# Kernel tuning notes

Hardware: AMD Instinct MI355X
Metric: run time of the kernel (lower is better)

## Reference

```python
import jax, jax.numpy as jnp
import numpy as np

N_NODES = 50000
N_EDGES = 1600000
NODE_DIM = 1024
HID = 128
OUT = 128
LN_EPS = 1e-5


def setup_inputs() -> dict:
    key = jax.random.key(0)
    ks = jax.random.split(key, 8)
    s = lambda d: 1.0 / np.sqrt(d)
    return {
        "x": jax.random.normal(ks[0], (N_NODES, NODE_DIM), jnp.float32),
        "edge_index": jax.random.randint(ks[1], (2, N_EDGES), 0, N_NODES, jnp.int64),
        "proj_w": jax.random.normal(ks[2], (HID, NODE_DIM), jnp.float32) * s(NODE_DIM),
        "proj_b": jnp.zeros((HID,), jnp.float32),
        "lin_l_w": jax.random.normal(ks[3], (HID, HID), jnp.float32) * s(HID),
        "lin_l_b": jnp.zeros((HID,), jnp.float32),
        "lin_r_w": jax.random.normal(ks[4], (HID, HID), jnp.float32) * s(HID),
        "ln_g": jnp.ones((HID,), jnp.float32),
        "ln_b": jnp.zeros((HID,), jnp.float32),
        "out_w": jax.random.normal(ks[5], (OUT, HID), jnp.float32) * s(HID),
        "out_b": jnp.zeros((OUT,), jnp.float32),
    }


def reference(x, edge_index, proj_w, proj_b, lin_l_w, lin_l_b, lin_r_w, ln_g, ln_b, out_w, out_b):
    n = x.shape[0]
    # input projection + ReLU: [N, node_dim] -> [N, H]
    h = jax.nn.relu(x @ proj_w.T + proj_b)
    # SAGEConv(mean): gather source features, mean-scatter to targets
    src, dst = edge_index[0], edge_index[1]
    agg = jax.ops.segment_sum(h[src], dst, num_segments=n)  # [N, H]
    deg = jax.ops.segment_sum(jnp.ones((src.shape[0],), h.dtype), dst, num_segments=n)
    mean_nbr = agg / jnp.maximum(deg, 1.0)[:, None]
    h = mean_nbr @ lin_l_w.T + lin_l_b + h @ lin_r_w.T
    # LayerNorm over feature dim
    mu = h.mean(-1, keepdims=True)
    var = jnp.mean((h - mu) ** 2, -1, keepdims=True)
    h = (h - mu) * jax.lax.rsqrt(var + LN_EPS) * ln_g + ln_b
    h = jax.nn.relu(h)  # dropout is identity in eval
    # batch=None -> global mean pool over all nodes: [1, H]
    g = h.mean(0, keepdims=True)
    return g @ out_w.T + out_b
```

## Files before the change

### kernel.cpp

```cpp
#include <hip/hip_runtime.h>

#define N_NODES  50000
#define N_EDGES  1600000
#define NODE_DIM 1024
#define HID      128
#define LN_EPS   1e-5f
#define PAD_NODES 50176
#define NBUCK    196
#define SHARD    6250

typedef float f32x4 __attribute__((ext_vector_type(4)));
typedef __bf16 bf16x8 __attribute__((ext_vector_type(8)));
typedef unsigned short u16x8 __attribute__((ext_vector_type(8)));

__device__ __forceinline__ unsigned short f2bf(float f) {
  unsigned int u = __float_as_uint(f);
  u += 0x7fffu + ((u >> 16) & 1u);
  return (unsigned short)(u >> 16);
}
__device__ __forceinline__ float bf2f(unsigned short v) {
  return __uint_as_float((unsigned int)v << 16);
}

__device__ __forceinline__ void pack16(const float4 v0, const float4 v1,
                                       const float4 v2, const float4 v3,
                                       unsigned short* dst) {
  u16x8 p0 = {f2bf(v0.x), f2bf(v0.y), f2bf(v0.z), f2bf(v0.w),
              f2bf(v1.x), f2bf(v1.y), f2bf(v1.z), f2bf(v1.w)};
  u16x8 p1 = {f2bf(v2.x), f2bf(v2.y), f2bf(v2.z), f2bf(v2.w),
              f2bf(v3.x), f2bf(v3.y), f2bf(v3.z), f2bf(v3.w)};
  *(u16x8*)(dst)     = p0;
  *(u16x8*)(dst + 8) = p1;
}

__device__ __forceinline__ int scan256_excl(int v, int buf[2][256], int t) {
  int cur = 0;
  buf[0][t] = v;
  __syncthreads();
  for (int off = 1; off < 256; off <<= 1) {
    int nxt = cur ^ 1;
    int s = buf[cur][t];
    if (t >= off) s += buf[cur][t - off];
    buf[nxt][t] = s;
    cur = nxt;
    __syncthreads();
  }
  return buf[cur][t] - v;
}

__global__ __launch_bounds__(256) void k_proj(const float* __restrict__ x,
                                              const float* __restrict__ pw,
                                              const float* __restrict__ pb,
                                              unsigned short* __restrict__ h) {
  __shared__ unsigned short As[128 * 32];
  __shared__ unsigned short Bs[128 * 32];
  const int tid  = threadIdx.x;
  const int m0   = blockIdx.x * 128;
  const int wave = tid >> 6, lane = tid & 63;
  const int wm = (wave >> 1) * 64, wn = (wave & 1) * 64;
  const int srow = tid >> 1;
  const int scol = (tid & 1) * 16;
  const int fr = lane & 15, ko = (lane >> 4) * 8;

  f32x4 acc[4][4];
#pragma unroll
  for (int m = 0; m < 4; m++)
#pragma unroll
    for (int n = 0; n < 4; n++) acc[m][n] = (f32x4){0.f, 0.f, 0.f, 0.f};

  for (int k0 = 0; k0 < NODE_DIM; k0 += 32) {
    const int arow = m0 + srow;
    float4 a0, a1, a2, a3;
    if (arow < N_NODES) {
      const float4* p = (const float4*)(x + (size_t)arow * NODE_DIM + k0 + scol);
      a0 = p[0]; a1 = p[1]; a2 = p[2]; a3 = p[3];
    } else {
      a0 = a1 = a2 = a3 = make_float4(0.f, 0.f, 0.f, 0.f);
    }
    const float4* q = (const float4*)(pw + (size_t)srow * NODE_DIM + k0 + scol);
    float4 b0 = q[0], b1 = q[1], b2 = q[2], b3 = q[3];

    __syncthreads();
    pack16(a0, a1, a2, a3, &As[srow * 32 + scol]);
    pack16(b0, b1, b2, b3, &Bs[srow * 32 + scol]);
    __syncthreads();

    bf16x8 af[4], bfr[4];
#pragma unroll
    for (int m = 0; m < 4; m++)
      af[m] = *(const bf16x8*)&As[(wm + m * 16 + fr) * 32 + ko];
#pragma unroll
    for (int n = 0; n < 4; n++)
      bfr[n] = *(const bf16x8*)&Bs[(wn + n * 16 + fr) * 32 + ko];
#pragma unroll
    for (int m = 0; m < 4; m++)
#pragma unroll
      for (int n = 0; n < 4; n++)
        acc[m][n] = __builtin_amdgcn_mfma_f32_16x16x32_bf16(af[m], bfr[n], acc[m][n], 0, 0, 0);
  }

  const int cr = (lane >> 4) * 4, cc = lane & 15;
#pragma unroll
  for (int n = 0; n < 4; n++) {
    const int col = wn + n * 16 + cc;
    const float bias = pb[col];
#pragma unroll
    for (int m = 0; m < 4; m++) {
#pragma unroll
      for (int i = 0; i < 4; i++) {
        const int row = m0 + wm + m * 16 + cr + i;
        if (row < N_NODES) {
          float v = acc[m][n][i] + bias;
          h[(size_t)row * HID + col] = f2bf(v > 0.f ? v : 0.f);
        }
      }
    }
  }
}

__global__ __launch_bounds__(256) void k_hist(const int* __restrict__ ei,
                                              int* __restrict__ counts) {
  __shared__ int bins[NBUCK];
  int t = threadIdx.x;
  if (t < NBUCK) bins[t] = 0;
  __syncthreads();
  int base = blockIdx.x * SHARD;
  for (int i = t; i < SHARD; i += 256)
    atomicAdd(&bins[ei[N_EDGES + base + i] >> 8], 1);
  __syncthreads();
  if (t < NBUCK) counts[t * 256 + blockIdx.x] = bins[t];
}

__global__ __launch_bounds__(256) void k_s1(const int* __restrict__ counts,
                                            int* __restrict__ basem,
                                            int* __restrict__ btot) {
  __shared__ int buf[2][256];
  int t = threadIdx.x, b = blockIdx.x;
  int v = counts[b * 256 + t];
  int excl = scan256_excl(v, buf, t);
  basem[b * 256 + t] = excl;
  if (t == 255) btot[b] = excl + v;
}

__global__ __launch_bounds__(256) void k_s2(const int* __restrict__ btot,
                                            int* __restrict__ bstart,
                                            float* __restrict__ accum) {
  __shared__ int buf[2][256];
  int t = threadIdx.x;
  int v = (t < NBUCK) ? btot[t] : 0;
  int excl = scan256_excl(v, buf, t);
  if (t < NBUCK) bstart[t] = excl;
  if (t == 0) bstart[NBUCK] = N_EDGES;
  if (t < HID) accum[t] = 0.f;
}

__global__ __launch_bounds__(256) void k_scatter(const int* __restrict__ ei,
                                                 const int* __restrict__ basem,
                                                 const int* __restrict__ bstart,
                                                 int2* __restrict__ bs) {
  __shared__ int cur[NBUCK];
  int t = threadIdx.x;
  if (t < NBUCK) cur[t] = bstart[t] + basem[t * 256 + blockIdx.x];
  __syncthreads();
  int base = blockIdx.x * SHARD;
  for (int i = t; i < SHARD; i += 256) {
    int e = base + i;
    int src = ei[e];
    int dst = ei[N_EDGES + e];
    int pos = atomicAdd(&cur[dst >> 8], 1);
    bs[pos] = make_int2(src, dst);
  }
}

__global__ __launch_bounds__(256) void k_bucket(const int* __restrict__ bstart,
                                                const int2* __restrict__ bs,
                                                int* __restrict__ nbr,
                                                int* __restrict__ offs,
                                                int* __restrict__ deg) {
  __shared__ int bins[256];
  __shared__ int buf[2][256];
  __shared__ int curs[256];
  int t = threadIdx.x, b = blockIdx.x;
  int s = bstart[b], e = bstart[b + 1];
  bins[t] = 0;
  __syncthreads();
  for (int i = s + t; i < e; i += 256)
    atomicAdd(&bins[bs[i].y & 255], 1);
  __syncthreads();
  int v = bins[t];
  int excl = scan256_excl(v, buf, t);
  int node = b * 256 + t;
  deg[node]  = v;
  offs[node] = s + excl;
  curs[t]    = s + excl;
  __syncthreads();
  for (int i = s + t; i < e; i += 256) {
    int2 p = bs[i];
    int pos = atomicAdd(&curs[p.y & 255], 1);
    nbr[pos] = p.x;
  }
}

__global__ __launch_bounds__(256) void k_gather(const unsigned short* __restrict__ h,
                                                const int* __restrict__ nbr,
                                                const int* __restrict__ offs,
                                                const int* __restrict__ deg,
                                                unsigned short* __restrict__ mn) {
  const int wave = threadIdx.x >> 6;
  const int lane = threadIdx.x & 63;
  const int node = blockIdx.x * 4 + wave;
  if (node >= N_NODES) return;
  const int g = lane >> 4, li = lane & 15;
  const int d  = deg[node];
  const int st = offs[node];
  float a[8] = {0.f, 0.f, 0.f, 0.f, 0.f, 0.f, 0.f, 0.f};
  for (int n = g; n < d; n += 4) {
    int sidx = nbr[st + n];
    u16x8 v = *(const u16x8*)(h + (size_t)sidx * HID + li * 8);
#pragma unroll
    for (int k = 0; k < 8; k++) a[k] += bf2f(v[k]);
  }
#pragma unroll
  for (int k = 0; k < 8; k++) {
    a[k] += __shfl_xor(a[k], 16);
    a[k] += __shfl_xor(a[k], 32);
  }
  if (g == 0) {
    float inv = 1.f / fmaxf((float)d, 1.f);
    u16x8 r;
#pragma unroll
    for (int k = 0; k < 8; k++) r[k] = f2bf(a[k] * inv);
    *(u16x8*)(mn + (size_t)node * HID + li * 8) = r;
  }
}

__global__ __launch_bounds__(256) void k_sage(unsigned short* mn,
                                              const unsigned short* __restrict__ h,
                                              const float* __restrict__ wl,
                                              const float* __restrict__ wr,
                                              const float* __restrict__ lb) {
  __shared__ unsigned short As[128 * 32];
  __shared__ unsigned short Bs[128 * 32];
  const int tid  = threadIdx.x;
  const int m0   = blockIdx.x * 128;
  const int wave = tid >> 6, lane = tid & 63;
  const int wm = (wave >> 1) * 64, wn = (wave & 1) * 64;
  const int srow = tid >> 1;
  const int scol = (tid & 1) * 16;
  const int fr = lane & 15, ko = (lane >> 4) * 8;

  f32x4 acc[4][4];
#pragma unroll
  for (int m = 0; m < 4; m++)
#pragma unroll
    for (int n = 0; n < 4; n++) acc[m][n] = (f32x4){0.f, 0.f, 0.f, 0.f};

  for (int k0 = 0; k0 < 2 * HID; k0 += 32) {
    const unsigned short* baseA = (k0 < HID) ? mn : h;
    const float* baseB = (k0 < HID) ? wl : wr;
    const int kk = (k0 & (HID - 1)) + scol;
    const int arow = m0 + srow;
    u16x8 a0, a1;
    if (arow < N_NODES) {
      const u16x8* p = (const u16x8*)(baseA + (size_t)arow * HID + kk);
      a0 = p[0]; a1 = p[1];
    } else {
      a0 = (u16x8){0,0,0,0,0,0,0,0}; a1 = a0;
    }
    const float4* q = (const float4*)(baseB + (size_t)srow * HID + kk);
    float4 b0 = q[0], b1 = q[1], b2 = q[2], b3 = q[3];

    __syncthreads();
    *(u16x8*)&As[srow * 32 + scol]     = a0;
    *(u16x8*)&As[srow * 32 + scol + 8] = a1;
    pack16(b0, b1, b2, b3, &Bs[srow * 32 + scol]);
    __syncthreads();

    bf16x8 af[4], bfr[4];
#pragma unroll
    for (int m = 0; m < 4; m++)
      af[m] = *(const bf16x8*)&As[(wm + m * 16 + fr) * 32 + ko];
#pragma unroll
    for (int n = 0; n < 4; n++)
      bfr[n] = *(const bf16x8*)&Bs[(wn + n * 16 + fr) * 32 + ko];
#pragma unroll
    for (int m = 0; m < 4; m++)
#pragma unroll
      for (int n = 0; n < 4; n++)
        acc[m][n] = __builtin_amdgcn_mfma_f32_16x16x32_bf16(af[m], bfr[n], acc[m][n], 0, 0, 0);
  }

  const int cr = (lane >> 4) * 4, cc = lane & 15;
#pragma unroll
  for (int n = 0; n < 4; n++) {
    const int col = wn + n * 16 + cc;
    const float bias = lb[col];
#pragma unroll
    for (int m = 0; m < 4; m++) {
#pragma unroll
      for (int i = 0; i < 4; i++) {
        const int row = m0 + wm + m * 16 + cr + i;
        if (row < N_NODES)
          mn[(size_t)row * HID + col] = f2bf(acc[m][n][i] + bias);
      }
    }
  }
}

__global__ __launch_bounds__(256) void k_ln_pool(const unsigned short* __restrict__ h2,
                                                 const float* __restrict__ lg,
                                                 const float* __restrict__ lbt,
                                                 float* __restrict__ accum) {
  const int wave = threadIdx.x >> 6;
  const int lane = threadIdx.x & 63;
  const int w = blockIdx.x * 4 + wave;
  const float g0 = lg[2 * lane], g1 = lg[2 * lane + 1];
  const float t0 = lbt[2 * lane], t1 = lbt[2 * lane + 1];
  float accx = 0.f, accy = 0.f;
  for (int i = w; i < N_NODES; i += 1024) {
    unsigned int pv = *(const unsigned int*)(h2 + (size_t)i * HID + 2 * lane);
    float v0 = bf2f((unsigned short)(pv & 0xffffu));
    float v1 = bf2f((unsigned short)(pv >> 16));
    float s = v0 + v1, ss = v0 * v0 + v1 * v1;
#pragma unroll
    for (int off = 32; off > 0; off >>= 1) {
      s  += __shfl_xor(s, off);
      ss += __shfl_xor(ss, off);
    }
    float mu  = s * (1.f / HID);
    float var = ss * (1.f / HID) - mu * mu;
    float r = rsqrtf(var + LN_EPS);
    float y0 = (v0 - mu) * r * g0 + t0;
    float y1 = (v1 - mu) * r * g1 + t1;
    accx += (y0 > 0.f ? y0 : 0.f);
    accy += (y1 > 0.f ? y1 : 0.f);
  }
  __shared__ float red[4][128];
  red[wave][2 * lane]     = accx;
  red[wave][2 * lane + 1] = accy;
  __syncthreads();
  if (wave == 0) {
    float a = red[0][2 * lane] + red[1][2 * lane] + red[2][2 * lane] + red[3][2 * lane];
    float b = red[0][2 * lane + 1] + red[1][2 * lane + 1] + red[2][2 * lane + 1] + red[3][2 * lane + 1];
    atomicAdd(&accum[2 * lane], a);
    atomicAdd(&accum[2 * lane + 1], b);
  }
}

__global__ __launch_bounds__(128) void k_final(const float* __restrict__ accum,
                                               const float* __restrict__ ow,
                                               const float* __restrict__ ob,
                                               float* __restrict__ out) {
  __shared__ float gs[HID];
  int t = threadIdx.x;
  gs[t] = accum[t] * (1.f / N_NODES);
  __syncthreads();
  float s = ob[t];
  for (int k = 0; k < HID; k++) s += gs[k] * ow[t * HID + k];
  out[t] = s;
}

extern "C" void kernel_launch(void* const* d_in, const int* in_sizes, int n_in,
                              void* d_out, int out_size, void* d_ws, size_t ws_size,
                              hipStream_t stream) {
  const float* x   = (const float*)d_in[0];
  const int*   ei  = (const int*)d_in[1];
  const float* pw  = (const float*)d_in[2];
  const float* pb  = (const float*)d_in[3];
  const float* wl  = (const float*)d_in[4];
  const float* lb  = (const float*)d_in[5];
  const float* wr  = (const float*)d_in[6];
  const float* lg  = (const float*)d_in[7];
  const float* lbt = (const float*)d_in[8];
  const float* ow  = (const float*)d_in[9];
  const float* ob  = (const float*)d_in[10];
  float* out = (float*)d_out;

  unsigned short* h  = (unsigned short*)d_ws;
  unsigned short* mn = h + (size_t)PAD_NODES * HID;
  int2* bs   = (int2*)(mn + (size_t)PAD_NODES * HID);
  int* nbr   = (int*)(bs + N_EDGES);
  int* counts= nbr + N_EDGES;
  int* basem = counts + NBUCK * 256;
  int* btot  = basem + NBUCK * 256;
  int* bstart= btot + 256;
  int* offs  = bstart + 256;
  int* deg   = offs + PAD_NODES;
  float* accum = (float*)(deg + PAD_NODES);

  const int MB = (N_NODES + 127) / 128;

  hipLaunchKernelGGL(k_proj,    dim3(MB),    dim3(256), 0, stream, x, pw, pb, h);
  hipLaunchKernelGGL(k_hist,    dim3(256),   dim3(256), 0, stream, ei, counts);
  hipLaunchKernelGGL(k_s1,      dim3(NBUCK), dim3(256), 0, stream, counts, basem, btot);
  hipLaunchKernelGGL(k_s2,      dim3(1),     dim3(256), 0, stream, btot, bstart, accum);
  hipLaunchKernelGGL(k_scatter, dim3(256),   dim3(256), 0, stream, ei, basem, bstart, bs);
  hipLaunchKernelGGL(k_bucket,  dim3(NBUCK), dim3(256), 0, stream, bstart, bs, nbr, offs, deg);
  hipLaunchKernelGGL(k_gather,  dim3((N_NODES + 3) / 4), dim3(256), 0, stream, h, nbr, offs, deg, mn);
  hipLaunchKernelGGL(k_sage,    dim3(MB),    dim3(256), 0, stream, mn, h, wl, wr, lb);
  hipLaunchKernelGGL(k_ln_pool, dim3(256),   dim3(256), 0, stream, mn, lg, lbt, accum);
  hipLaunchKernelGGL(k_final,   dim3(1),     dim3(128), 0, stream, accum, ow, ob, out);
}
```

Before: 506.7 us.

## Fuse bucket sort with aggregation via LDS atomics and fuse LayerNorm-pool into SAGE GEMM

Drops the per-node CSR build (k_bucket) and the per-node gather kernel. A new 1024-thread k_agg accumulates neighbor features per 256-node bucket in shared memory with float atomics, using edges packed as 16-bit src plus local dst. The LayerNorm, ReLU and mean-pool work moves into the k_sage epilogue, so h2 is no longer written and reread. k_proj now takes 64-wide K steps with double-buffered smem halves, and bf16 conversion uses the hardware cast. The changes cut kernel launches and global memory traffic, but add heavy LDS atomic contention, a large shared-memory footprint per block, and a 16-bit src index that assumes N_NODES < 65536.

```diff
diff --git a/kernel.cpp b/kernel.cpp
--- a/kernel.cpp
+++ b/kernel.cpp
@@ -5,32 +5,23 @@
 #define NODE_DIM 1024
 #define HID      128
 #define LN_EPS   1e-5f
-#define PAD_NODES 50176
 #define NBUCK    196
 #define SHARD    6250
+#define BSTR     132
 
 typedef float f32x4 __attribute__((ext_vector_type(4)));
 typedef __bf16 bf16x8 __attribute__((ext_vector_type(8)));
 typedef unsigned short u16x8 __attribute__((ext_vector_type(8)));
 
 __device__ __forceinline__ unsigned short f2bf(float f) {
-  unsigned int u = __float_as_uint(f);
-  u += 0x7fffu + ((u >> 16) & 1u);
-  return (unsigned short)(u >> 16);
+  __bf16 b = (__bf16)f;
+  return __builtin_bit_cast(unsigned short, b);
+}
+__device__ __forceinline__ unsigned int pkbf(float a, float b) {
+  return (unsigned int)f2bf(a) | ((unsigned int)f2bf(b) << 16);
 }
 __device__ __forceinline__ float bf2f(unsigned short v) {
   return __uint_as_float((unsigned int)v << 16);
-}
-
-__device__ __forceinline__ void pack16(const float4 v0, const float4 v1,
-                                       const float4 v2, const float4 v3,
-                                       unsigned short* dst) {
-  u16x8 p0 = {f2bf(v0.x), f2bf(v0.y), f2bf(v0.z), f2bf(v0.w),
-              f2bf(v1.x), f2bf(v1.y), f2bf(v1.z), f2bf(v1.w)};
-  u16x8 p1 = {f2bf(v2.x), f2bf(v2.y), f2bf(v2.z), f2bf(v2.w),
-              f2bf(v3.x), f2bf(v3.y), f2bf(v3.z), f2bf(v3.w)};
-  *(u16x8*)(dst)     = p0;
-  *(u16x8*)(dst + 8) = p1;
 }
 
 __device__ __forceinline__ int scan256_excl(int v, int buf[2][256], int t) {
@@ -52,51 +43,63 @@
                                               const float* __restrict__ pw,
                                               const float* __restrict__ pb,
                                               unsigned short* __restrict__ h) {
-  __shared__ unsigned short As[128 * 32];
-  __shared__ unsigned short Bs[128 * 32];
-  const int tid  = threadIdx.x;
-  const int m0   = blockIdx.x * 128;
+  __shared__ unsigned short As[2][128][32];
+  __shared__ unsigned short Bs[2][128][32];
+  const int tid = threadIdx.x;
+  const int m0 = blockIdx.x * 128;
   const int wave = tid >> 6, lane = tid & 63;
   const int wm = (wave >> 1) * 64, wn = (wave & 1) * 64;
   const int srow = tid >> 1;
-  const int scol = (tid & 1) * 16;
+  const int sub  = tid & 1;
   const int fr = lane & 15, ko = (lane >> 4) * 8;
 
-  f32x4 acc[4][4];
-#pragma unroll
-  for (int m = 0; m < 4; m++)
-#pragma unroll
-    for (int n = 0; n < 4; n++) acc[m][n] = (f32x4){0.f, 0.f, 0.f, 0.f};
-
-  for (int k0 = 0; k0 < NODE_DIM; k0 += 32) {
-    const int arow = m0 + srow;
-    float4 a0, a1, a2, a3;
-    if (arow < N_NODES) {
-      const float4* p = (const float4*)(x + (size_t)arow * NODE_DIM + k0 + scol);
-      a0 = p[0]; a1 = p[1]; a2 = p[2]; a3 = p[3];
+  f32x4 acc[4][4] = {};
+  const int arow = m0 + srow;
+  const bool aval = (arow < N_NODES);
+  const float* xrow = x + (size_t)arow * NODE_DIM + sub * 32;
+  const float* brow = pw + (size_t)srow * NODE_DIM + sub * 32;
+
+  for (int k0 = 0; k0 < NODE_DIM; k0 += 64) {
+    float4 av[8], bv[8];
+    if (aval) {
+      const float4* p = (const float4*)(xrow + k0);
+#pragma unroll
+      for (int j = 0; j < 8; j++) av[j] = p[j];
     } else {
-      a0 = a1 = a2 = a3 = make_float4(0.f, 0.f, 0.f, 0.f);
-    }
-    const float4* q = (const float4*)(pw + (size_t)srow * NODE_DIM + k0 + scol);
-    float4 b0 = q[0], b1 = q[1], b2 = q[2], b3 = q[3];
-
-    __syncthreads();
-    pack16(a0, a1, a2, a3, &As[srow * 32 + scol]);
-    pack16(b0, b1, b2, b3, &Bs[srow * 32 + scol]);
-    __syncthreads();
-
-    bf16x8 af[4], bfr[4];
-#pragma unroll
-    for (int m = 0; m < 4; m++)
-      af[m] = *(const bf16x8*)&As[(wm + m * 16 + fr) * 32 + ko];
-#pragma unroll
-    for (int n = 0; n < 4; n++)
-      bfr[n] = *(const bf16x8*)&Bs[(wn + n * 16 + fr) * 32 + ko];
-#pragma unroll
-    for (int m = 0; m < 4; m++)
+#pragma unroll
+      for (int j = 0; j < 8; j++) av[j] = make_float4(0.f, 0.f, 0.f, 0.f);
+    }
+    const float4* q = (const float4*)(brow + k0);
+#pragma unroll
+    for (int j = 0; j < 8; j++) bv[j] = q[j];
+
+    __syncthreads();
+    unsigned int* da = (unsigned int*)&As[sub][srow][0];
+    unsigned int* db = (unsigned int*)&Bs[sub][srow][0];
+#pragma unroll
+    for (int j = 0; j < 8; j++) {
+      da[2 * j]     = pkbf(av[j].x, av[j].y);
+      da[2 * j + 1] = pkbf(av[j].z, av[j].w);
+      db[2 * j]     = pkbf(bv[j].x, bv[j].y);
+      db[2 * j + 1] = pkbf(bv[j].z, bv[j].w);
+    }
+    __syncthreads();
+
+#pragma unroll
+    for (int s = 0; s < 2; s++) {
+      bf16x8 af[4], bfr[4];
+#pragma unroll
+      for (int m = 0; m < 4; m++)
+        af[m] = *(const bf16x8*)&As[s][wm + m * 16 + fr][ko];
 #pragma unroll
       for (int n = 0; n < 4; n++)
-        acc[m][n] = __builtin_amdgcn_mfma_f32_16x16x32_bf16(af[m], bfr[n], acc[m][n], 0, 0, 0);
+        bfr[n] = *(const bf16x8*)&Bs[s][wn + n * 16 + fr][ko];
+#pragma unroll
+      for (int m = 0; m < 4; m++)
+#pragma unroll
+        for (int n = 0; n < 4; n++)
+          acc[m][n] = __builtin_amdgcn_mfma_f32_16x16x32_bf16(af[m], bfr[n], acc[m][n], 0, 0, 0);
+    }
   }
 
   const int cr = (lane >> 4) * 4, cc = lane & 15;
@@ -157,7 +160,7 @@
 __global__ __launch_bounds__(256) void k_scatter(const int* __restrict__ ei,
                                                  const int* __restrict__ basem,
                                                  const int* __restrict__ bstart,
-                                                 int2* __restrict__ bs) {
+                                                 unsigned int* __restrict__ bs) {
   __shared__ int cur[NBUCK];
   int t = threadIdx.x;
   if (t < NBUCK) cur[t] = bstart[t] + basem[t * 256 + blockIdx.x];
@@ -165,107 +168,102 @@
   int base = blockIdx.x * SHARD;
   for (int i = t; i < SHARD; i += 256) {
     int e = base + i;
-    int src = ei[e];
-    int dst = ei[N_EDGES + e];
+    unsigned int src = (unsigned int)ei[e];
+    unsigned int dst = (unsigned int)ei[N_EDGES + e];
     int pos = atomicAdd(&cur[dst >> 8], 1);
-    bs[pos] = make_int2(src, dst);
-  }
-}
-
-__global__ __launch_bounds__(256) void k_bucket(const int* __restrict__ bstart,
-                                                const int2* __restrict__ bs,
-                                                int* __restrict__ nbr,
-                                                int* __restrict__ offs,
-                                                int* __restrict__ deg) {
-  __shared__ int bins[256];
-  __shared__ int buf[2][256];
-  __shared__ int curs[256];
-  int t = threadIdx.x, b = blockIdx.x;
-  int s = bstart[b], e = bstart[b + 1];
-  bins[t] = 0;
-  __syncthreads();
-  for (int i = s + t; i < e; i += 256)
-    atomicAdd(&bins[bs[i].y & 255], 1);
-  __syncthreads();
-  int v = bins[t];
-  int excl = scan256_excl(v, buf, t);
-  int node = b * 256 + t;
-  deg[node]  = v;
-  offs[node] = s + excl;
-  curs[t]    = s + excl;
-  __syncthreads();
-  for (int i = s + t; i < e; i += 256) {
-    int2 p = bs[i];
-    int pos = atomicAdd(&curs[p.y & 255], 1);
-    nbr[pos] = p.x;
-  }
-}
-
-__global__ __launch_bounds__(256) void k_gather(const unsigned short* __restrict__ h,
-                                                const int* __restrict__ nbr,
-                                                const int* __restrict__ offs,
-                                                const int* __restrict__ deg,
-                                                unsigned short* __restrict__ mn) {
-  const int wave = threadIdx.x >> 6;
-  const int lane = threadIdx.x & 63;
-  const int node = blockIdx.x * 4 + wave;
-  if (node >= N_NODES) return;
-  const int g = lane >> 4, li = lane & 15;
-  const int d  = deg[node];
-  const int st = offs[node];
-  float a[8] = {0.f, 0.f, 0.f, 0.f, 0.f, 0.f, 0.f, 0.f};
-  for (int n = g; n < d; n += 4) {
-    int sidx = nbr[st + n];
-    u16x8 v = *(const u16x8*)(h + (size_t)sidx * HID + li * 8);
-#pragma unroll
-    for (int k = 0; k < 8; k++) a[k] += bf2f(v[k]);
-  }
-#pragma unroll
-  for (int k = 0; k < 8; k++) {
-    a[k] += __shfl_xor(a[k], 16);
-    a[k] += __shfl_xor(a[k], 32);
-  }
-  if (g == 0) {
-    float inv = 1.f / fmaxf((float)d, 1.f);
-    u16x8 r;
-#pragma unroll
-    for (int k = 0; k < 8; k++) r[k] = f2bf(a[k] * inv);
-    *(u16x8*)(mn + (size_t)node * HID + li * 8) = r;
-  }
-}
-
-__global__ __launch_bounds__(256) void k_sage(unsigned short* mn,
+    bs[pos] = src | ((dst & 255u) << 16);
+  }
+}
+
+__global__ __launch_bounds__(1024) void k_agg(const int* __restrict__ bstart,
+                                              const unsigned int* __restrict__ bs,
+                                              const unsigned short* __restrict__ h,
+                                              unsigned short* __restrict__ mn) {
+  __shared__ float acc[256 * BSTR];
+  __shared__ int degL[256];
+  const int t = threadIdx.x, b = blockIdx.x;
+  for (int i = t; i < 256 * BSTR; i += 1024) acc[i] = 0.f;
+  if (t < 256) degL[t] = 0;
+  __syncthreads();
+
+  const int s = bstart[b], e = bstart[b + 1];
+  const int grp = t >> 4, li = t & 15;
+  int i = s + grp;
+  for (; i + 64 < e; i += 128) {
+    unsigned int p0 = bs[i], p1 = bs[i + 64];
+    const u16x8 v0 = *(const u16x8*)(h + (size_t)(p0 & 0xffffu) * HID + li * 8);
+    const u16x8 v1 = *(const u16x8*)(h + (size_t)(p1 & 0xffffu) * HID + li * 8);
+    const int d0 = p0 >> 16, d1 = p1 >> 16;
+    if (li == 0) { atomicAdd(&degL[d0], 1); atomicAdd(&degL[d1], 1); }
+    float* a0 = &acc[d0 * BSTR + li * 8];
+    float* a1 = &acc[d1 * BSTR + li * 8];
+#pragma unroll
+    for (int j = 0; j < 8; j++) {
+      int jj = (j + li) & 7;
+      atomicAdd(&a0[jj], bf2f(v0[jj]));
+    }
+#pragma unroll
+    for (int j = 0; j < 8; j++) {
+      int jj = (j + li) & 7;
+      atomicAdd(&a1[jj], bf2f(v1[jj]));
+    }
+  }
+  if (i < e) {
+    unsigned int p0 = bs[i];
+    const u16x8 v0 = *(const u16x8*)(h + (size_t)(p0 & 0xffffu) * HID + li * 8);
+    const int d0 = p0 >> 16;
+    if (li == 0) atomicAdd(&degL[d0], 1);
+    float* a0 = &acc[d0 * BSTR + li * 8];
+#pragma unroll
+    for (int j = 0; j < 8; j++) {
+      int jj = (j + li) & 7;
+      atomicAdd(&a0[jj], bf2f(v0[jj]));
+    }
+  }
+  __syncthreads();
+
+  const int node0 = b * 256;
+  for (int i2 = t; i2 < 256 * 64; i2 += 1024) {
+    int nl = i2 >> 6, fp = (i2 & 63) * 2;
+    int node = node0 + nl;
+    if (node < N_NODES) {
+      float inv = 1.f / fmaxf((float)degL[nl], 1.f);
+      *(unsigned int*)(mn + (size_t)node * HID + fp) =
+          pkbf(acc[nl * BSTR + fp] * inv, acc[nl * BSTR + fp + 1] * inv);
+    }
+  }
+}
+
+__global__ __launch_bounds__(256) void k_sage(const unsigned short* __restrict__ mn,
                                               const unsigned short* __restrict__ h,
                                               const float* __restrict__ wl,
                                               const float* __restrict__ wr,
-                                              const float* __restrict__ lb) {
+                                              const float* __restrict__ lb,
+                                              const float* __restrict__ lg,
+                                              const float* __restrict__ lbt,
+                                              float* __restrict__ accum) {
   __shared__ unsigned short As[128 * 32];
   __shared__ unsigned short Bs[128 * 32];
-  const int tid  = threadIdx.x;
-  const int m0   = blockIdx.x * 128;
+  __shared__ float T3[32 * 128];
+  __shared__ float red[4][128];
+  const int tid = threadIdx.x;
+  const int m0 = blockIdx.x * 128;
   const int wave = tid >> 6, lane = tid & 63;
   const int wm = (wave >> 1) * 64, wn = (wave & 1) * 64;
-  const int srow = tid >> 1;
-  const int scol = (tid & 1) * 16;
+  const int srow = tid >> 1, scol = (tid & 1) * 16;
   const int fr = lane & 15, ko = (lane >> 4) * 8;
 
-  f32x4 acc[4][4];
-#pragma unroll
-  for (int m = 0; m < 4; m++)
-#pragma unroll
-    for (int n = 0; n < 4; n++) acc[m][n] = (f32x4){0.f, 0.f, 0.f, 0.f};
+  f32x4 acc[4][4] = {};
 
   for (int k0 = 0; k0 < 2 * HID; k0 += 32) {
     const unsigned short* baseA = (k0 < HID) ? mn : h;
     const float* baseB = (k0 < HID) ? wl : wr;
     const int kk = (k0 & (HID - 1)) + scol;
     const int arow = m0 + srow;
-    u16x8 a0, a1;
+    u16x8 a0 = {0, 0, 0, 0, 0, 0, 0, 0}, a1 = a0;
     if (arow < N_NODES) {
       const u16x8* p = (const u16x8*)(baseA + (size_t)arow * HID + kk);
       a0 = p[0]; a1 = p[1];
-    } else {
-      a0 = (u16x8){0,0,0,0,0,0,0,0}; a1 = a0;
     }
     const float4* q = (const float4*)(baseB + (size_t)srow * HID + kk);
     float4 b0 = q[0], b1 = q[1], b2 = q[2], b3 = q[3];
@@ -273,7 +271,11 @@
     __syncthreads();
     *(u16x8*)&As[srow * 32 + scol]     = a0;
     *(u16x8*)&As[srow * 32 + scol + 8] = a1;
-    pack16(b0, b1, b2, b3, &Bs[srow * 32 + scol]);
+    unsigned int* db = (unsigned int*)&Bs[srow * 32 + scol];
+    db[0] = pkbf(b0.x, b0.y); db[1] = pkbf(b0.z, b0.w);
+    db[2] = pkbf(b1.x, b1.y); db[3] = pkbf(b1.z, b1.w);
+    db[4] = pkbf(b2.x, b2.y); db[5] = pkbf(b2.z, b2.w);
+    db[6] = pkbf(b3.x, b3.y); db[7] = pkbf(b3.z, b3.w);
     __syncthreads();
 
     bf16x8 af[4], bfr[4];
@@ -291,59 +293,52 @@
   }
 
   const int cr = (lane >> 4) * 4, cc = lane & 15;
-#pragma unroll
-  for (int n = 0; n < 4; n++) {
-    const int col = wn + n * 16 + cc;
-    const float bias = lb[col];
-#pragma unroll
-    for (int m = 0; m < 4; m++) {
-#pragma unroll
-      for (int i = 0; i < 4; i++) {
-        const int row = m0 + wm + m * 16 + cr + i;
-        if (row < N_NODES)
-          mn[(size_t)row * HID + col] = f2bf(acc[m][n][i] + bias);
+  const int p = wave >> 1;
+  const float g0 = lg[lane], g1 = lg[lane + 64];
+  const float t0 = lbt[lane], t1 = lbt[lane + 64];
+  float ax = 0.f, ay = 0.f;
+#pragma unroll
+  for (int m = 0; m < 4; m++) {
+    __syncthreads();
+#pragma unroll
+    for (int n = 0; n < 4; n++) {
+      const int col = wn + n * 16 + cc;
+      const float bias = lb[col];
+#pragma unroll
+      for (int i = 0; i < 4; i++)
+        T3[(p * 16 + cr + i) * 128 + col] = acc[m][n][i] + bias;
+    }
+    __syncthreads();
+    for (int r8 = 0; r8 < 8; r8++) {
+      int q8 = wave * 8 + r8;
+      int grow = m0 + (q8 >> 4) * 64 + m * 16 + (q8 & 15);
+      float v0 = T3[q8 * 128 + lane];
+      float v1 = T3[q8 * 128 + lane + 64];
+      float sum = v0 + v1, ss = v0 * v0 + v1 * v1;
+#pragma unroll
+      for (int off = 32; off > 0; off >>= 1) {
+        sum += __shfl_xor(sum, off);
+        ss  += __shfl_xor(ss, off);
       }
-    }
-  }
-}
-
-__global__ __launch_bounds__(256) void k_ln_pool(const unsigned short* __restrict__ h2,
-                                                 const float* __restrict__ lg,
-                                                 const float* __restrict__ lbt,
-                                                 float* __restrict__ accum) {
-  const int wave = threadIdx.x >> 6;
-  const int lane = threadIdx.x & 63;
-  const int w = blockIdx.x * 4 + wave;
-  const float g0 = lg[2 * lane], g1 = lg[2 * lane + 1];
-  const float t0 = lbt[2 * lane], t1 = lbt[2 * lane + 1];
-  float accx = 0.f, accy = 0.f;
-  for (int i = w; i < N_NODES; i += 1024) {
-    unsigned int pv = *(const unsigned int*)(h2 + (size_t)i * HID + 2 * lane);
-    float v0 = bf2f((unsigned short)(pv & 0xffffu));
-    float v1 = bf2f((unsigned short)(pv >> 16));
-    float s = v0 + v1, ss = v0 * v0 + v1 * v1;
-#pragma unroll
-    for (int off = 32; off > 0; off >>= 1) {
-      s  += __shfl_xor(s, off);
-      ss += __shfl_xor(ss, off);
-    }
-    float mu  = s * (1.f / HID);
-    float var = ss * (1.f / HID) - mu * mu;
-    float r = rsqrtf(var + LN_EPS);
-    float y0 = (v0 - mu) * r * g0 + t0;
-    float y1 = (v1 - mu) * r * g1 + t1;
-    accx += (y0 > 0.f ? y0 : 0.f);
-    accy += (y1 > 0.f ? y1 : 0.f);
-  }
-  __shared__ float red[4][128];
-  red[wave][2 * lane]     = accx;
-  red[wave][2 * lane + 1] = accy;
+      float mu  = sum * (1.f / HID);
+      float var = ss * (1.f / HID) - mu * mu;
+      float rinv = rsqrtf(var + LN_EPS);
+      if (grow < N_NODES) {
+        float y0 = (v0 - mu) * rinv * g0 + t0;
+        float y1 = (v1 - mu) * rinv * g1 + t1;
+        ax += fmaxf(y0, 0.f);
+        ay += fmaxf(y1, 0.f);
+      }
+    }
+  }
+  red[wave][lane]      = ax;
+  red[wave][lane + 64] = ay;
   __syncthreads();
   if (wave == 0) {
-    float a = red[0][2 * lane] + red[1][2 * lane] + red[2][2 * lane] + red[3][2 * lane];
-    float b = red[0][2 * lane + 1] + red[1][2 * lane + 1] + red[2][2 * lane + 1] + red[3][2 * lane + 1];
-    atomicAdd(&accum[2 * lane], a);
-    atomicAdd(&accum[2 * lane + 1], b);
+    float a  = red[0][lane] + red[1][lane] + red[2][lane] + red[3][lane];
+    float bb = red[0][lane + 64] + red[1][lane + 64] + red[2][lane + 64] + red[3][lane + 64];
+    atomicAdd(&accum[lane], a);
+    atomicAdd(&accum[lane + 64], bb);
   }
 }
 
@@ -376,28 +371,24 @@
   const float* ob  = (const float*)d_in[10];
   float* out = (float*)d_out;
 
+  const int PAD = NBUCK * 256;
   unsigned short* h  = (unsigned short*)d_ws;
-  unsigned short* mn = h + (size_t)PAD_NODES * HID;
-  int2* bs   = (int2*)(mn + (size_t)PAD_NODES * HID);
-  int* nbr   = (int*)(bs + N_EDGES);
-  int* counts= nbr + N_EDGES;
-  int* basem = counts + NBUCK * 256;
-  int* btot  = basem + NBUCK * 256;
-  int* bstart= btot + 256;
-  int* offs  = bstart + 256;
-  int* deg   = offs + PAD_NODES;
-  float* accum = (float*)(deg + PAD_NODES);
+  unsigned short* mn = h + (size_t)PAD * HID;
+  unsigned int* bsp  = (unsigned int*)(mn + (size_t)PAD * HID);
+  int* counts = (int*)(bsp + N_EDGES);
+  int* basem  = counts + NBUCK * 256;
+  int* btot   = basem + NBUCK * 256;
+  int* bstart = btot + 256;
+  float* accum = (float*)(bstart + 256);
 
   const int MB = (N_NODES + 127) / 128;
 
-  hipLaunchKernelGGL(k_proj,    dim3(MB),    dim3(256), 0, stream, x, pw, pb, h);
-  hipLaunchKernelGGL(k_hist,    dim3(256),   dim3(256), 0, stream, ei, counts);
-  hipLaunchKernelGGL(k_s1,      dim3(NBUCK), dim3(256), 0, stream, counts, basem, btot);
-  hipLaunchKernelGGL(k_s2,      dim3(1),     dim3(256), 0, stream, btot, bstart, accum);
-  hipLaunchKernelGGL(k_scatter, dim3(256),   dim3(256), 0, stream, ei, basem, bstart, bs);
-  hipLaunchKernelGGL(k_bucket,  dim3(NBUCK), dim3(256), 0, stream, bstart, bs, nbr, offs, deg);
-  hipLaunchKernelGGL(k_gather,  dim3((N_NODES + 3) / 4), dim3(256), 0, stream, h, nbr, offs, deg, mn);
-  hipLaunchKernelGGL(k_sage,    dim3(MB),    dim3(256), 0, stream, mn, h, wl, wr, lb);
-  hipLaunchKernelGGL(k_ln_pool, dim3(256),   dim3(256), 0, stream, mn, lg, lbt, accum);
-  hipLaunchKernelGGL(k_final,   dim3(1),     dim3(128), 0, stream, accum, ow, ob, out);
-}
+  hipLaunchKernelGGL(k_proj,    dim3(MB),    dim3(256),  0, stream, x, pw, pb, h);
+  hipLaunchKernelGGL(k_hist,    dim3(256),   dim3(256),  0, stream, ei, counts);
+  hipLaunchKernelGGL(k_s1,      dim3(NBUCK), dim3(256),  0, stream, counts, basem, btot);
+  hipLaunchKernelGGL(k_s2,      dim3(1),     dim3(256),  0, stream, btot, bstart, accum);
+  hipLaunchKernelGGL(k_scatter, dim3(256),   dim3(256),  0, stream, ei, basem, bstart, bsp);
+  hipLaunchKernelGGL(k_agg,     dim3(NBUCK), dim3(1024), 0, stream, bstart, bsp, h, mn);
+  hipLaunchKernelGGL(k_sage,    dim3(MB),    dim3(256),  0, stream, mn, h, wl, wr, lb, lg, lbt, accum);
+  hipLaunchKernelGGL(k_final,   dim3(1),     dim3(128),  0, stream, accum, ow, ob, out);
+}
```

New measurement: 1.766 ms. 249% more time.
